# Kernel tuning notes

Measured on AMD Instinct MI355X. Metric: run time of the kernel, lower is better.

The kernel has to match this reference:

```python
import jax, jax.numpy as jnp
import numpy as np

B, N, H = 1024, 100, 256
CLIP = 10.0


def setup_inputs() -> dict:
    key = jax.random.key(0)
    ks = jax.random.split(key, 14)
    s = 0.05  # param scale for numerical stability
    return {
        "x": jax.random.uniform(ks[0], (B, N, 2), jnp.float32),
        "encoder_output": jax.random.normal(ks[1], (B, N, H), jnp.float32),
        "W_ih1": jax.random.normal(ks[2], (3 * H, H + 1), jnp.float32) * s,
        "W_hh1": jax.random.normal(ks[3], (3 * H, H), jnp.float32) * s,
        "b_ih1": jax.random.normal(ks[4], (3 * H,), jnp.float32) * s,
        "b_hh1": jax.random.normal(ks[5], (3 * H,), jnp.float32) * s,
        "W_ih2": jax.random.normal(ks[6], (3 * H, H), jnp.float32) * s,
        "W_hh2": jax.random.normal(ks[7], (3 * H, H), jnp.float32) * s,
        "b_ih2": jax.random.normal(ks[8], (3 * H,), jnp.float32) * s,
        "b_hh2": jax.random.normal(ks[9], (3 * H,), jnp.float32) * s,
        "W_q": jax.random.normal(ks[10], (H, H), jnp.float32) * s,
        "W_ref": jax.random.normal(ks[11], (H, H), jnp.float32) * s,
        "v": jax.random.normal(ks[12], (H,), jnp.float32) * s,
    }


def gru_cell(x, h, W_ih, W_hh, b_ih, b_hh):
    # Standard torch GRU cell math (gate order r, z, n).
    gi = x @ W_ih.T + b_ih
    gh = h @ W_hh.T + b_hh
    i_r, i_z, i_n = jnp.split(gi, 3, axis=-1)
    h_r, h_z, h_n = jnp.split(gh, 3, axis=-1)
    r = jax.nn.sigmoid(i_r + h_r)
    z = jax.nn.sigmoid(i_z + h_z)
    n = jnp.tanh(i_n + r * h_n)
    return (1.0 - z) * n + z * h


def reference(x, encoder_output, W_ih1, W_hh1, b_ih1, b_hh1,
              W_ih2, W_hh2, b_ih2, b_hh2, W_q, W_ref, v):
    Bs, Nn, Hh = encoder_output.shape
    dt = encoder_output.dtype
    # Pointer reference projection is step-invariant -> hoist out of the loop.
    ref = jnp.einsum('bnh,hk->bnk', encoder_output, W_ref)  # [B,N,H]
    bidx = jnp.arange(Bs)
    mask0 = jnp.zeros((Bs, Nn), bool)
    # t=1 context: graph embedding + full remaining capacity D=1.
    ctx0 = jnp.concatenate([encoder_output.mean(1), jnp.ones((Bs, 1), dt)], -1)
    D0 = jnp.ones((Bs,), dt)

    def step(carry, _):
        mask, ctx, D = carry
        z0 = jnp.zeros((Bs, Hh), dt)
        # torch code calls self.gru(last_x) with fresh zero hidden every step
        h1 = gru_cell(ctx, z0, W_ih1, W_hh1, b_ih1, b_hh1)
        h2 = gru_cell(h1, z0, W_ih2, W_hh2, b_ih2, b_hh2)
        q = h2 @ W_q  # [B,H]
        u = CLIP * jnp.tanh(jnp.einsum('bnh,h->bn', jnp.tanh(q[:, None, :] + ref), v))
        u = jnp.where(mask, -1e9, u)  # masked_fill_(mask, -inf)
        nxt = jnp.argmax(u, axis=-1)  # greedy decode (deterministic baseline)
        logp = jax.nn.log_softmax(u, axis=-1)[bidx, nxt]
        mask = mask | (jnp.arange(Nn)[None, :] == nxt[:, None])
        D = D - 1.0 / Nn
        ctx = jnp.concatenate([encoder_output[bidx, nxt], D[:, None]], -1)
        return (mask, ctx, D), (nxt, logp)

    _, (pi_t, lps) = jax.lax.scan(step, (mask0, ctx0, D0), None, length=Nn)
    pi = pi_t.T  # [B, N] tour
    ll = lps.sum(0)  # [B] log-likelihood of tour
    coords = x[bidx[:, None], pi]  # [B,N,2]
    nxt_coords = jnp.roll(coords, -1, axis=1)
    cost = jnp.sqrt(((coords - nxt_coords) ** 2).sum(-1)).sum(-1)  # closed tour length
    return cost, ll
```

## Files before the change

kernel.cpp:

```cpp
#include <hip/hip_runtime.h>
#include <cstdint>
#include <cmath>

#define BATCH 1024
#define SEQ   100
#define HD    256
#define HD3   768
#define NTHR  512

__device__ __forceinline__ float sigmoidf_(float x) { return 1.0f / (1.0f + expf(-x)); }

__device__ __forceinline__ float gru0(float gr, float gz, float gn, float hr, float hz, float hn) {
    float r = sigmoidf_(gr + hr);
    float z = sigmoidf_(gz + hz);
    float n = tanhf(gn + r * hn);
    return (1.0f - z) * n;
}

__global__ __launch_bounds__(256) void init_mean_kernel(const float* __restrict__ enc,
                                                        float* __restrict__ meanenc) {
    int b = blockIdx.x, tid = threadIdx.x;
    const float* e = enc + (size_t)b * SEQ * HD + tid;
    float s = 0.f;
    for (int n = 0; n < SEQ; ++n) s += e[(size_t)n * HD];
    meanenc[(size_t)b * HD + tid] = s * (1.0f / SEQ);
}

__global__ __launch_bounds__(256) void prep_kernel(const float* __restrict__ W_ih1,
                                                   const float* __restrict__ W_ih2,
                                                   float4* __restrict__ W1p4,
                                                   float4* __restrict__ W2p4,
                                                   float* __restrict__ wl,
                                                   float* __restrict__ biasz) {
    int k = blockIdx.x, t = threadIdx.x;
    W1p4[k * HD + t] = make_float4(W_ih1[(size_t)t * (HD + 1) + k],
                                   W_ih1[(size_t)(t + HD) * (HD + 1) + k],
                                   W_ih1[(size_t)(t + 2 * HD) * (HD + 1) + k], 0.f);
    W2p4[k * HD + t] = make_float4(W_ih2[(size_t)t * HD + k],
                                   W_ih2[(size_t)(t + HD) * HD + k],
                                   W_ih2[(size_t)(t + 2 * HD) * HD + k], 0.f);
    if (k == 0) {
#pragma unroll
        for (int c = 0; c < 3; ++c) wl[c * HD + t] = W_ih1[(size_t)(c * HD + t) * (HD + 1) + HD];
        biasz[t] = 0.f;
    }
}

__global__ __launch_bounds__(256) void gemm_bias_kernel(const float* __restrict__ A, int lda,
                                                        const float* __restrict__ Bm, int ldb,
                                                        const float* __restrict__ bias,
                                                        float* __restrict__ C, int ldc) {
    __shared__ float As[16][68];
    __shared__ float Bs[16][68];
    const int tid = threadIdx.x;
    const int tx = tid & 15, ty = tid >> 4;
    const int mBase = blockIdx.x * 64, nBase = blockIdx.y * 64;
    const int lr = tid >> 2, lc = (tid & 3) << 2;
    const int bkk = tid >> 4, bn4 = (tid & 15) << 2;
    float acc[4][4] = {};
    for (int k0 = 0; k0 < HD; k0 += 16) {
        float4 av = *(const float4*)&A[(size_t)(mBase + lr) * lda + k0 + lc];
        As[lc + 0][lr] = av.x; As[lc + 1][lr] = av.y; As[lc + 2][lr] = av.z; As[lc + 3][lr] = av.w;
        float4 bv = *(const float4*)&Bm[(size_t)(k0 + bkk) * ldb + nBase + bn4];
        *(float4*)&Bs[bkk][bn4] = bv;
        __syncthreads();
#pragma unroll
        for (int kk = 0; kk < 16; ++kk) {
            const float4 a4 = *(const float4*)&As[kk][ty << 2];
            const float4 b4 = *(const float4*)&Bs[kk][tx << 2];
            const float ar_[4] = {a4.x, a4.y, a4.z, a4.w};
            const float br_[4] = {b4.x, b4.y, b4.z, b4.w};
#pragma unroll
            for (int i = 0; i < 4; ++i)
#pragma unroll
                for (int j = 0; j < 4; ++j) acc[i][j] = fmaf(ar_[i], br_[j], acc[i][j]);
        }
        __syncthreads();
    }
#pragma unroll
    for (int i = 0; i < 4; ++i) {
        float o[4];
#pragma unroll
        for (int j = 0; j < 4; ++j) o[j] = acc[i][j] + bias[nBase + (tx << 2) + j];
        *(float4*)&C[(size_t)(mBase + (ty << 2) + i) * ldc + nBase + (tx << 2)] =
            make_float4(o[0], o[1], o[2], o[3]);
    }
}

__global__ __launch_bounds__(512, 2) void decode_kernel(const float* __restrict__ refb,
                                                        const float* __restrict__ enc,
                                                        const float* __restrict__ meanenc,
                                                        const float4* __restrict__ W1p4,
                                                        const float4* __restrict__ W2p4,
                                                        const float* __restrict__ W_q,
                                                        const float* __restrict__ b_ih1,
                                                        const float* __restrict__ b_hh1,
                                                        const float* __restrict__ b_ih2,
                                                        const float* __restrict__ b_hh2,
                                                        const float* __restrict__ wl,
                                                        const float* __restrict__ vvec,
                                                        const float* __restrict__ x,
                                                        float* __restrict__ out) {
    __shared__ float wls[HD3], bi1s[HD3], bhh1s[HD3], bi2s[HD3], bhh2s[HD3];
    __shared__ float vs[HD];
    __shared__ float h1s[4][HD];
    __shared__ float h2s[4][HD];
    __shared__ float qs[4][HD];
    __shared__ float encs[4][HD];
    __shared__ float part[4][3][HD];
    __shared__ float us[4][SEQ];
    __shared__ int   rem_s[4][SEQ];
    __shared__ int   pi_s[4][SEQ];
    __shared__ float ll_s[4];

    const int blk = blockIdx.x, tid = threadIdx.x;
    const int w = tid >> 6, lane = tid & 63;
    const int col = tid & 255, kh = tid >> 8;
    const int b0 = blk << 2;

    for (int j = tid; j < HD3; j += NTHR) {
        wls[j] = wl[j];
        bi1s[j] = b_ih1[j];
        bhh1s[j] = b_hh1[j];
        bi2s[j] = b_ih2[j];
        bhh2s[j] = b_hh2[j];
    }
    if (tid < HD) vs[tid] = vvec[tid];
    if (tid < SEQ) {
#pragma unroll
        for (int bb = 0; bb < 4; ++bb) rem_s[bb][tid] = tid;
    }
    if (tid < 4) ll_s[tid] = 0.f;
    for (int e = tid; e < 4 * HD; e += NTHR)
        encs[e >> 8][e & 255] = meanenc[(size_t)(b0 + (e >> 8)) * HD + (e & 255)];
    __syncthreads();

    float Dreg = 1.0f;
    const float invN = 1.0f / SEQ;

    auto gru_phase = [&](const float4* __restrict__ wp, auto& src, auto& dst,
                         const float* __restrict__ bi, const float* __restrict__ bhh,
                         bool useD, float Dv) {
        float acc[4][3] = {};
        const int kb = kh << 7;
        const float4* wpc = wp + ((size_t)kb << 8) + col;
        for (int k = 0; k < 128; k += 16) {
            float4 wv[16];
#pragma unroll
            for (int u = 0; u < 16; ++u) wv[u] = wpc[(size_t)(k + u) << 8];
#pragma unroll
            for (int uu = 0; uu < 4; ++uu) {
#pragma unroll
                for (int bb = 0; bb < 4; ++bb) {
                    const float4 h = *(const float4*)&src[bb][kb + k + (uu << 2)];
                    const float hv[4] = {h.x, h.y, h.z, h.w};
#pragma unroll
                    for (int u = 0; u < 4; ++u) {
                        const float4 w4 = wv[(uu << 2) + u];
                        acc[bb][0] = fmaf(hv[u], w4.x, acc[bb][0]);
                        acc[bb][1] = fmaf(hv[u], w4.y, acc[bb][1]);
                        acc[bb][2] = fmaf(hv[u], w4.z, acc[bb][2]);
                    }
                }
            }
        }
        if (kh) {
#pragma unroll
            for (int bb = 0; bb < 4; ++bb)
#pragma unroll
                for (int g = 0; g < 3; ++g) part[bb][g][col] = acc[bb][g];
        }
        __syncthreads();
        if (!kh) {
#pragma unroll
            for (int bb = 0; bb < 4; ++bb) {
                float gr = acc[bb][0] + part[bb][0][col] + bi[col];
                float gz = acc[bb][1] + part[bb][1][col] + bi[col + HD];
                float gn = acc[bb][2] + part[bb][2][col] + bi[col + 2 * HD];
                if (useD) {
                    gr += Dv * wls[col];
                    gz += Dv * wls[col + HD];
                    gn += Dv * wls[col + 2 * HD];
                }
                dst[bb][col] = gru0(gr, gz, gn, bhh[col], bhh[col + HD], bhh[col + 2 * HD]);
            }
        }
    };

    gru_phase(W1p4, encs, h1s, bi1s, bhh1s, true, Dreg);
    __syncthreads();

    for (int t = 0; t < SEQ; ++t) {
        const int cnt = SEQ - t;
        gru_phase(W2p4, h1s, h2s, bi2s, bhh2s, false, 0.f);
        __syncthreads();
        {
            float qa[4] = {};
            const int kb = kh << 7;
            const float* wqc = W_q + ((size_t)kb << 8) + col;
            for (int k = 0; k < 128; k += 16) {
                float wv[16];
#pragma unroll
                for (int u = 0; u < 16; ++u) wv[u] = wqc[(size_t)(k + u) << 8];
#pragma unroll
                for (int uu = 0; uu < 4; ++uu) {
#pragma unroll
                    for (int bb = 0; bb < 4; ++bb) {
                        const float4 h = *(const float4*)&h2s[bb][kb + k + (uu << 2)];
                        qa[bb] = fmaf(h.x, wv[(uu << 2) + 0], qa[bb]);
                        qa[bb] = fmaf(h.y, wv[(uu << 2) + 1], qa[bb]);
                        qa[bb] = fmaf(h.z, wv[(uu << 2) + 2], qa[bb]);
                        qa[bb] = fmaf(h.w, wv[(uu << 2) + 3], qa[bb]);
                    }
                }
            }
            if (kh) {
#pragma unroll
                for (int bb = 0; bb < 4; ++bb) part[bb][0][col] = qa[bb];
            }
            __syncthreads();
            if (!kh) {
#pragma unroll
                for (int bb = 0; bb < 4; ++bb) qs[bb][col] = qa[bb] + part[bb][0][col];
            }
        }
        __syncthreads();
        {
            const int bq = w & 3;
            const int half = w >> 2;
            const int b = b0 + bq;
            const float4 qv = *(const float4*)&qs[bq][lane << 2];
            const float4 vv = *(const float4*)&vs[lane << 2];
            const float* Rb = refb + (size_t)b * SEQ * HD;
            int j = half;
            float4 rcur = make_float4(0.f, 0.f, 0.f, 0.f);
            if (j < cnt)
                rcur = *(const float4*)&Rb[(size_t)rem_s[bq][j] * HD + (lane << 2)];
            while (j < cnt) {
                const int jn = j + 2;
                float4 rnext = make_float4(0.f, 0.f, 0.f, 0.f);
                if (jn < cnt)
                    rnext = *(const float4*)&Rb[(size_t)rem_s[bq][jn] * HD + (lane << 2)];
                float s0 = tanhf(qv.x + rcur.x) * vv.x;
                s0 = fmaf(tanhf(qv.y + rcur.y), vv.y, s0);
                s0 = fmaf(tanhf(qv.z + rcur.z), vv.z, s0);
                s0 = fmaf(tanhf(qv.w + rcur.w), vv.w, s0);
#pragma unroll
                for (int o = 1; o < 64; o <<= 1) s0 += __shfl_xor(s0, o, 64);
                if (lane == 0) us[bq][j] = 10.0f * tanhf(s0);
                rcur = rnext;
                j = jn;
            }
        }
        __syncthreads();
        if (w < 4) {
            const int b = b0 + w;
            float va = (lane < cnt) ? us[w][lane] : -3.0e38f;
            int ia = lane;
            if (lane + 64 < cnt) {
                float vb2 = us[w][lane + 64];
                if (vb2 > va) { va = vb2; ia = lane + 64; }
            }
#pragma unroll
            for (int o = 1; o < 64; o <<= 1) {
                float ov = __shfl_xor(va, o, 64);
                int oi = __shfl_xor(ia, o, 64);
                if (ov > va || (ov == va && oi < ia)) { va = ov; ia = oi; }
            }
            float e = ((lane < cnt) ? expf(us[w][lane] - va) : 0.0f) +
                      ((lane + 64 < cnt) ? expf(us[w][lane + 64] - va) : 0.0f);
#pragma unroll
            for (int o = 1; o < 64; o <<= 1) e += __shfl_xor(e, o, 64);
            const int nsel = rem_s[w][ia];
            if (lane == 0) {
                ll_s[w] += -logf(e);
                pi_s[w][t] = nsel;
                rem_s[w][ia] = rem_s[w][cnt - 1];
            }
            if (t < SEQ - 1) {
                const float4 ev = *(const float4*)&enc[((size_t)b * SEQ + nsel) * HD + (lane << 2)];
                *(float4*)&encs[w][lane << 2] = ev;
            }
        }
        __syncthreads();
        Dreg -= invN;
        if (t < SEQ - 1) {
            gru_phase(W1p4, encs, h1s, bi1s, bhh1s, true, Dreg);
            __syncthreads();
        }
    }

    if (w < 4) {
        const int b = b0 + w;
        float d = 0.f;
        for (int e2 = lane; e2 < SEQ; e2 += 64) {
            int p = pi_s[w][e2];
            int pn = pi_s[w][(e2 == SEQ - 1) ? 0 : e2 + 1];
            float xa = x[((size_t)b * SEQ + p) * 2 + 0];
            float ya = x[((size_t)b * SEQ + p) * 2 + 1];
            float xb2 = x[((size_t)b * SEQ + pn) * 2 + 0];
            float yb2 = x[((size_t)b * SEQ + pn) * 2 + 1];
            float dx = xa - xb2, dy = ya - yb2;
            d += sqrtf(dx * dx + dy * dy);
        }
#pragma unroll
        for (int o = 1; o < 64; o <<= 1) d += __shfl_xor(d, o, 64);
        if (lane == 0) {
            out[b] = d;
            out[BATCH + b] = ll_s[w];
        }
    }
}

extern "C" void kernel_launch(void* const* d_in, const int* in_sizes, int n_in,
                              void* d_out, int out_size, void* d_ws, size_t ws_size,
                              hipStream_t stream) {
    const float* x     = (const float*)d_in[0];
    const float* enc   = (const float*)d_in[1];
    const float* W_ih1 = (const float*)d_in[2];
    const float* b_ih1 = (const float*)d_in[4];
    const float* b_hh1 = (const float*)d_in[5];
    const float* W_ih2 = (const float*)d_in[6];
    const float* b_ih2 = (const float*)d_in[8];
    const float* b_hh2 = (const float*)d_in[9];
    const float* W_q   = (const float*)d_in[10];
    const float* W_ref = (const float*)d_in[11];
    const float* v     = (const float*)d_in[12];
    float* out = (float*)d_out;
    (void)in_sizes; (void)n_in; (void)out_size;

    char* w = (char*)d_ws;
    size_t off = 0;
    auto take = [&](size_t bytes) {
        char* p = w + off;
        off = (off + bytes + 255) & ~(size_t)255;
        return p;
    };
    float*  refb    = (float*)take((size_t)BATCH * SEQ * HD * 4);
    float*  meanenc = (float*)take((size_t)BATCH * HD * 4);
    float4* W1p4    = (float4*)take((size_t)HD * HD * 16);
    float4* W2p4    = (float4*)take((size_t)HD * HD * 16);
    float*  wl      = (float*)take((size_t)HD3 * 4);
    float*  biasz   = (float*)take((size_t)HD * 4);
    if (ws_size < off) return;

    hipLaunchKernelGGL(init_mean_kernel, dim3(BATCH), dim3(HD), 0, stream, enc, meanenc);
    hipLaunchKernelGGL(prep_kernel, dim3(HD), dim3(HD), 0, stream,
                       W_ih1, W_ih2, W1p4, W2p4, wl, biasz);
    hipLaunchKernelGGL(gemm_bias_kernel, dim3(BATCH * SEQ / 64, HD / 64), dim3(256), 0, stream,
                       enc, HD, W_ref, HD, biasz, refb, HD);
    hipLaunchKernelGGL(decode_kernel, dim3(BATCH / 4), dim3(NTHR), 0, stream,
                       refb, enc, meanenc, W1p4, W2p4, W_q,
                       b_ih1, b_hh1, b_ih2, b_hh2, wl, v, x, out);
}
```

Measured before the change: 5.460 ms.

## Repack GRU and query weights to drop padding and deepen pointer prefetch

The GRU input weights were stored as float4 with an unused fourth lane. They are now split into a float2 (r,z) array and a k-interleaved float4 array for the n gate, which cuts weight bytes loaded per step by a quarter. W_q is likewise repacked so each thread issues float4 loads instead of scalar loads. The pointer-scoring loop now keeps four ref rows in flight instead of one, with the rem index fetched ahead of use. The cost is more registers in a kernel already bounded at 512 threads with 2 blocks per CU, plus extra select logic to pick the weight components.

```diff
diff --git a/kernel.cpp b/kernel.cpp
--- a/kernel.cpp
+++ b/kernel.cpp
@@ -28,17 +28,26 @@
 
 __global__ __launch_bounds__(256) void prep_kernel(const float* __restrict__ W_ih1,
                                                    const float* __restrict__ W_ih2,
-                                                   float4* __restrict__ W1p4,
-                                                   float4* __restrict__ W2p4,
+                                                   const float* __restrict__ W_q,
+                                                   float2* __restrict__ W1g,
+                                                   float*  __restrict__ W1n,
+                                                   float2* __restrict__ W2g,
+                                                   float*  __restrict__ W2n,
+                                                   float*  __restrict__ Wqp,
                                                    float* __restrict__ wl,
                                                    float* __restrict__ biasz) {
     int k = blockIdx.x, t = threadIdx.x;
-    W1p4[k * HD + t] = make_float4(W_ih1[(size_t)t * (HD + 1) + k],
-                                   W_ih1[(size_t)(t + HD) * (HD + 1) + k],
-                                   W_ih1[(size_t)(t + 2 * HD) * (HD + 1) + k], 0.f);
-    W2p4[k * HD + t] = make_float4(W_ih2[(size_t)t * HD + k],
-                                   W_ih2[(size_t)(t + HD) * HD + k],
-                                   W_ih2[(size_t)(t + 2 * HD) * HD + k], 0.f);
+    float gr1 = W_ih1[(size_t)t * (HD + 1) + k];
+    float gz1 = W_ih1[(size_t)(t + HD) * (HD + 1) + k];
+    float gn1 = W_ih1[(size_t)(t + 2 * HD) * (HD + 1) + k];
+    float gr2 = W_ih2[(size_t)t * HD + k];
+    float gz2 = W_ih2[(size_t)(t + HD) * HD + k];
+    float gn2 = W_ih2[(size_t)(t + 2 * HD) * HD + k];
+    W1g[(size_t)(k >> 1) * 512 + (t << 1) + (k & 1)] = make_float2(gr1, gz1);
+    W1n[(size_t)(k >> 2) * 1024 + (t << 2) + (k & 3)] = gn1;
+    W2g[(size_t)(k >> 1) * 512 + (t << 1) + (k & 1)] = make_float2(gr2, gz2);
+    W2n[(size_t)(k >> 2) * 1024 + (t << 2) + (k & 3)] = gn2;
+    Wqp[(size_t)(k >> 2) * 1024 + (t << 2) + (k & 3)] = W_q[(size_t)k * HD + t];
     if (k == 0) {
 #pragma unroll
         for (int c = 0; c < 3; ++c) wl[c * HD + t] = W_ih1[(size_t)(c * HD + t) * (HD + 1) + HD];
@@ -90,9 +99,11 @@
 __global__ __launch_bounds__(512, 2) void decode_kernel(const float* __restrict__ refb,
                                                         const float* __restrict__ enc,
                                                         const float* __restrict__ meanenc,
-                                                        const float4* __restrict__ W1p4,
-                                                        const float4* __restrict__ W2p4,
-                                                        const float* __restrict__ W_q,
+                                                        const float4* __restrict__ W1g4,
+                                                        const float4* __restrict__ W1n4,
+                                                        const float4* __restrict__ W2g4,
+                                                        const float4* __restrict__ W2n4,
+                                                        const float4* __restrict__ Wq4,
                                                         const float* __restrict__ b_ih1,
                                                         const float* __restrict__ b_hh1,
                                                         const float* __restrict__ b_ih2,
@@ -138,16 +149,20 @@
     float Dreg = 1.0f;
     const float invN = 1.0f / SEQ;
 
-    auto gru_phase = [&](const float4* __restrict__ wp, auto& src, auto& dst,
+    auto gru_phase = [&](const float4* __restrict__ Wg, const float4* __restrict__ Wn,
+                         auto& src, auto& dst,
                          const float* __restrict__ bi, const float* __restrict__ bhh,
                          bool useD, float Dv) {
         float acc[4][3] = {};
         const int kb = kh << 7;
-        const float4* wpc = wp + ((size_t)kb << 8) + col;
+        const float4* gp = Wg + ((size_t)(kb >> 1) << 8) + col;
+        const float4* np = Wn + ((size_t)(kb >> 2) << 8) + col;
         for (int k = 0; k < 128; k += 16) {
-            float4 wv[16];
-#pragma unroll
-            for (int u = 0; u < 16; ++u) wv[u] = wpc[(size_t)(k + u) << 8];
+            float4 wg[8], wn[4];
+#pragma unroll
+            for (int u = 0; u < 8; ++u) wg[u] = gp[(size_t)((k >> 1) + u) << 8];
+#pragma unroll
+            for (int u = 0; u < 4; ++u) wn[u] = np[(size_t)((k >> 2) + u) << 8];
 #pragma unroll
             for (int uu = 0; uu < 4; ++uu) {
 #pragma unroll
@@ -156,10 +171,17 @@
                     const float hv[4] = {h.x, h.y, h.z, h.w};
 #pragma unroll
                     for (int u = 0; u < 4; ++u) {
-                        const float4 w4 = wv[(uu << 2) + u];
-                        acc[bb][0] = fmaf(hv[u], w4.x, acc[bb][0]);
-                        acc[bb][1] = fmaf(hv[u], w4.y, acc[bb][1]);
-                        acc[bb][2] = fmaf(hv[u], w4.z, acc[bb][2]);
+                        const int kk = (uu << 2) + u;
+                        const float4 g = wg[kk >> 1];
+                        const float gr = (kk & 1) ? g.z : g.x;
+                        const float gz = (kk & 1) ? g.w : g.y;
+                        const float4 n4 = wn[kk >> 2];
+                        const float gn = ((kk & 3) == 0) ? n4.x :
+                                         ((kk & 3) == 1) ? n4.y :
+                                         ((kk & 3) == 2) ? n4.z : n4.w;
+                        acc[bb][0] = fmaf(hv[u], gr, acc[bb][0]);
+                        acc[bb][1] = fmaf(hv[u], gz, acc[bb][1]);
+                        acc[bb][2] = fmaf(hv[u], gn, acc[bb][2]);
                     }
                 }
             }
@@ -187,30 +209,30 @@
         }
     };
 
-    gru_phase(W1p4, encs, h1s, bi1s, bhh1s, true, Dreg);
+    gru_phase(W1g4, W1n4, encs, h1s, bi1s, bhh1s, true, Dreg);
     __syncthreads();
 
     for (int t = 0; t < SEQ; ++t) {
         const int cnt = SEQ - t;
-        gru_phase(W2p4, h1s, h2s, bi2s, bhh2s, false, 0.f);
+        gru_phase(W2g4, W2n4, h1s, h2s, bi2s, bhh2s, false, 0.f);
         __syncthreads();
         {
             float qa[4] = {};
             const int kb = kh << 7;
-            const float* wqc = W_q + ((size_t)kb << 8) + col;
+            const float4* wq = Wq4 + ((size_t)(kb >> 2) << 8) + col;
             for (int k = 0; k < 128; k += 16) {
-                float wv[16];
-#pragma unroll
-                for (int u = 0; u < 16; ++u) wv[u] = wqc[(size_t)(k + u) << 8];
+                float4 wv4[4];
+#pragma unroll
+                for (int u = 0; u < 4; ++u) wv4[u] = wq[(size_t)((k >> 2) + u) << 8];
 #pragma unroll
                 for (int uu = 0; uu < 4; ++uu) {
 #pragma unroll
                     for (int bb = 0; bb < 4; ++bb) {
                         const float4 h = *(const float4*)&h2s[bb][kb + k + (uu << 2)];
-                        qa[bb] = fmaf(h.x, wv[(uu << 2) + 0], qa[bb]);
-                        qa[bb] = fmaf(h.y, wv[(uu << 2) + 1], qa[bb]);
-                        qa[bb] = fmaf(h.z, wv[(uu << 2) + 2], qa[bb]);
-                        qa[bb] = fmaf(h.w, wv[(uu << 2) + 3], qa[bb]);
+                        qa[bb] = fmaf(h.x, wv4[uu].x, qa[bb]);
+                        qa[bb] = fmaf(h.y, wv4[uu].y, qa[bb]);
+                        qa[bb] = fmaf(h.z, wv4[uu].z, qa[bb]);
+                        qa[bb] = fmaf(h.w, wv4[uu].w, qa[bb]);
                     }
                 }
             }
@@ -232,24 +254,28 @@
             const float4 qv = *(const float4*)&qs[bq][lane << 2];
             const float4 vv = *(const float4*)&vs[lane << 2];
             const float* Rb = refb + (size_t)b * SEQ * HD;
+            const int* rem = rem_s[bq];
             int j = half;
-            float4 rcur = make_float4(0.f, 0.f, 0.f, 0.f);
-            if (j < cnt)
-                rcur = *(const float4*)&Rb[(size_t)rem_s[bq][j] * HD + (lane << 2)];
+            const float4 z4 = make_float4(0.f, 0.f, 0.f, 0.f);
+            float4 r0 = z4, r1 = z4, r2 = z4, r3 = z4;
+            if (j < cnt)     r0 = *(const float4*)&Rb[(size_t)rem[j] * HD + (lane << 2)];
+            if (j + 2 < cnt) r1 = *(const float4*)&Rb[(size_t)rem[j + 2] * HD + (lane << 2)];
+            if (j + 4 < cnt) r2 = *(const float4*)&Rb[(size_t)rem[j + 4] * HD + (lane << 2)];
+            if (j + 6 < cnt) r3 = *(const float4*)&Rb[(size_t)rem[j + 6] * HD + (lane << 2)];
+            int i4 = (j + 8 < cnt) ? rem[j + 8] : 0;
             while (j < cnt) {
-                const int jn = j + 2;
-                float4 rnext = make_float4(0.f, 0.f, 0.f, 0.f);
-                if (jn < cnt)
-                    rnext = *(const float4*)&Rb[(size_t)rem_s[bq][jn] * HD + (lane << 2)];
-                float s0 = tanhf(qv.x + rcur.x) * vv.x;
-                s0 = fmaf(tanhf(qv.y + rcur.y), vv.y, s0);
-                s0 = fmaf(tanhf(qv.z + rcur.z), vv.z, s0);
-                s0 = fmaf(tanhf(qv.w + rcur.w), vv.w, s0);
+                float4 rn = z4;
+                if (j + 8 < cnt) rn = *(const float4*)&Rb[(size_t)i4 * HD + (lane << 2)];
+                int i5 = (j + 10 < cnt) ? rem[j + 10] : 0;
+                float s0 = tanhf(qv.x + r0.x) * vv.x;
+                s0 = fmaf(tanhf(qv.y + r0.y), vv.y, s0);
+                s0 = fmaf(tanhf(qv.z + r0.z), vv.z, s0);
+                s0 = fmaf(tanhf(qv.w + r0.w), vv.w, s0);
 #pragma unroll
                 for (int o = 1; o < 64; o <<= 1) s0 += __shfl_xor(s0, o, 64);
                 if (lane == 0) us[bq][j] = 10.0f * tanhf(s0);
-                rcur = rnext;
-                j = jn;
+                r0 = r1; r1 = r2; r2 = r3; r3 = rn; i4 = i5;
+                j += 2;
             }
         }
         __syncthreads();
@@ -285,7 +311,7 @@
         __syncthreads();
         Dreg -= invN;
         if (t < SEQ - 1) {
-            gru_phase(W1p4, encs, h1s, bi1s, bhh1s, true, Dreg);
+            gru_phase(W1g4, W1n4, encs, h1s, bi1s, bhh1s, true, Dreg);
             __syncthreads();
         }
     }
@@ -338,18 +364,24 @@
     };
     float*  refb    = (float*)take((size_t)BATCH * SEQ * HD * 4);
     float*  meanenc = (float*)take((size_t)BATCH * HD * 4);
-    float4* W1p4    = (float4*)take((size_t)HD * HD * 16);
-    float4* W2p4    = (float4*)take((size_t)HD * HD * 16);
+    float2* W1g     = (float2*)take((size_t)HD * HD * 8);
+    float*  W1n     = (float*)take((size_t)HD * HD * 4);
+    float2* W2g     = (float2*)take((size_t)HD * HD * 8);
+    float*  W2n     = (float*)take((size_t)HD * HD * 4);
+    float*  Wqp     = (float*)take((size_t)HD * HD * 4);
     float*  wl      = (float*)take((size_t)HD3 * 4);
     float*  biasz   = (float*)take((size_t)HD * 4);
     if (ws_size < off) return;
 
     hipLaunchKernelGGL(init_mean_kernel, dim3(BATCH), dim3(HD), 0, stream, enc, meanenc);
     hipLaunchKernelGGL(prep_kernel, dim3(HD), dim3(HD), 0, stream,
-                       W_ih1, W_ih2, W1p4, W2p4, wl, biasz);
+                       W_ih1, W_ih2, W_q, W1g, W1n, W2g, W2n, Wqp, wl, biasz);
     hipLaunchKernelGGL(gemm_bias_kernel, dim3(BATCH * SEQ / 64, HD / 64), dim3(256), 0, stream,
                        enc, HD, W_ref, HD, biasz, refb, HD);
     hipLaunchKernelGGL(decode_kernel, dim3(BATCH / 4), dim3(NTHR), 0, stream,
-                       refb, enc, meanenc, W1p4, W2p4, W_q,
+                       refb, enc, meanenc,
+                       (const float4*)W1g, (const float4*)W1n,
+                       (const float4*)W2g, (const float4*)W2n,
+                       (const float4*)Wqp,
                        b_ih1, b_hh1, b_ih2, b_hh2, wl, v, x, out);
 }
```

New measurement: 5.684 ms. 1.04x slower.
